# Optimization experiments

Hardware: AMD Instinct MI355X
Metric: run time of the kernel (lower is better)

The kernel has to match this reference:

```python
import jax, jax.numpy as jnp
import numpy as np

N = 50000          # nodes
E = 800000         # edges (before self-loops)
IN_CH = 128
H1, C1 = 8, 32     # layer-1 heads / channels-per-head (concat -> 256)
H2, C2 = 1, 64     # layer-2 (out_channels=64, heads=1)
NEG_SLOPE = 0.2    # PyG GATConv default LeakyReLU slope for attention


def setup_inputs() -> dict:
    key = jax.random.key(0)
    ks = jax.random.split(key, 10)
    x = jax.random.normal(ks[0], (N, IN_CH), dtype=jnp.float32)
    edge_index = jax.random.randint(ks[1], (2, E), 0, N, dtype=jnp.int64)
    s = 0.05
    W1 = jax.random.normal(ks[2], (IN_CH, H1 * C1), dtype=jnp.float32) * s
    a_src1 = jax.random.normal(ks[3], (H1, C1), dtype=jnp.float32) * s
    a_dst1 = jax.random.normal(ks[4], (H1, C1), dtype=jnp.float32) * s
    b1 = jnp.zeros((H1 * C1,), dtype=jnp.float32)
    W2 = jax.random.normal(ks[5], (H1 * C1, H2 * C2), dtype=jnp.float32) * s
    a_src2 = jax.random.normal(ks[6], (H2, C2), dtype=jnp.float32) * s
    a_dst2 = jax.random.normal(ks[7], (H2, C2), dtype=jnp.float32) * s
    b2 = jnp.zeros((H2 * C2,), dtype=jnp.float32)
    return {"x": x, "edge_index": edge_index,
            "W1": W1, "a_src1": a_src1, "a_dst1": a_dst1, "b1": b1,
            "W2": W2, "a_src2": a_src2, "a_dst2": a_dst2, "b2": b2}


def gat_conv(x, src, dst, W, a_src, a_dst, b, heads, ch):
    """PyG GATConv (eval mode): gather -> LeakyReLU attn -> scatter-softmax -> scatter-add."""
    n = x.shape[0]
    h = (x @ W).reshape(n, heads, ch)                     # [N, H, C]
    alpha_s = jnp.einsum('nhc,hc->nh', h, a_src)          # [N, H]
    alpha_d = jnp.einsum('nhc,hc->nh', h, a_dst)
    e = jax.nn.leaky_relu(alpha_s[src] + alpha_d[dst], NEG_SLOPE)  # [E, H]
    # numerically-stable softmax over edges grouped by destination node
    emax = jax.ops.segment_max(e, dst, num_segments=n)
    e = jnp.exp(e - emax[dst])
    denom = jax.ops.segment_sum(e, dst, num_segments=n)
    alpha = e / denom[dst]                                # [E, H]
    out = jax.ops.segment_sum(h[src] * alpha[:, :, None], dst, num_segments=n)  # [N, H, C]
    return out.reshape(n, heads * ch) + b


def reference(x, edge_index, W1, a_src1, a_dst1, b1, W2, a_src2, a_dst2, b2):
    # PyG GATConv adds self-loops by default
    loops = jnp.arange(N, dtype=edge_index.dtype)
    src = jnp.concatenate([edge_index[0], loops])
    dst = jnp.concatenate([edge_index[1], loops])
    h = jax.nn.relu(gat_conv(x, src, dst, W1, a_src1, a_dst1, b1, H1, C1))
    out = jax.nn.relu(gat_conv(h, src, dst, W2, a_src2, a_dst2, b2, H2, C2))
    return out
```

## Files before the change

kernel.cpp:

```cpp
#include <hip/hip_runtime.h>
#include <math.h>

#define NEG_SLOPE 0.2f
__device__ __forceinline__ float leaky(float x) { return fmaxf(x, NEG_SLOPE * x); }

typedef _Float16 f16;
typedef _Float16 f16x4 __attribute__((ext_vector_type(4)));
typedef _Float16 f16x8 __attribute__((ext_vector_type(8)));
typedef float f32x4 __attribute__((ext_vector_type(4)));

__device__ __forceinline__ int kmap(int lh, int e) {
  return (e < 4) ? lh * 4 + e : 16 + lh * 4 + (e - 4);
}

__global__ void k_count(const int* __restrict__ dst, int* __restrict__ deg,
                        int* __restrict__ rank, int E) {
  int e = blockIdx.x * blockDim.x + threadIdx.x;
  if (e < E) {
    int d = dst[e];
    rank[e] = atomicAdd(&deg[d], 1);
  }
}

#define W1_TOT (17 * 4 * 64 * 8)
#define W2_TOT (5 * 8 * 64 * 8)
__global__ __launch_bounds__(256) void k_partial_packw(const int* __restrict__ deg,
    int* __restrict__ part, int n, int nb,
    const float* __restrict__ W1, const float* __restrict__ as1f,
    const float* __restrict__ ad1f, const float* __restrict__ W2,
    const float* __restrict__ as2f, const float* __restrict__ ad2f,
    f16* __restrict__ Wp1, f16* __restrict__ Wp2) {
  if ((int)blockIdx.x < nb) {
    __shared__ int s[256];
    int i = blockIdx.x * 256 + threadIdx.x;
    s[threadIdx.x] = (i < n) ? deg[i] : 0;
    __syncthreads();
    for (int off = 128; off > 0; off >>= 1) {
      if (threadIdx.x < off) s[threadIdx.x] += s[threadIdx.x + off];
      __syncthreads();
    }
    if (threadIdx.x == 0) part[blockIdx.x] = s[0];
  }
  int tid = blockIdx.x * 256 + threadIdx.x;
  if (tid < W1_TOT) {
    int e = tid & 7, l = (tid >> 3) & 63, ks = (tid >> 9) & 3, nt = tid >> 11;
    int lh = l >> 4, li = l & 15;
    int k = ks * 32 + kmap(lh, e);
    float v;
    if (nt < 16) {
      v = W1[k * 256 + nt * 16 + li];
    } else {
      int h = li & 7;
      const float* a = (li < 8) ? (as1f + h * 32) : (ad1f + h * 32);
      v = 0.f;
      for (int j = 0; j < 32; ++j) v += W1[k * 256 + h * 32 + j] * a[j];
    }
    Wp1[tid] = (f16)v;
  } else if (tid < W1_TOT + W2_TOT) {
    int t2 = tid - W1_TOT;
    int e = t2 & 7, l = (t2 >> 3) & 63, ks = (t2 >> 9) & 7, nt = t2 >> 12;
    int lh = l >> 4, li = l & 15;
    int k = ks * 32 + kmap(lh, e);
    float v = 0.f;
    if (nt < 4) {
      v = W2[k * 64 + nt * 16 + li];
    } else if (li == 0) {
      for (int j = 0; j < 64; ++j) v += W2[k * 64 + j] * as2f[j];
    } else if (li == 1) {
      for (int j = 0; j < 64; ++j) v += W2[k * 64 + j] * ad2f[j];
    }
    Wp2[t2] = (f16)v;
  }
}

__global__ __launch_bounds__(256) void k_offs(const int* __restrict__ deg,
                                              const int* __restrict__ part,
                                              int* __restrict__ offs, int n, int nb) {
  __shared__ int ps[256];
  __shared__ int s[256];
  int t = threadIdx.x;
  ps[t] = (t < nb) ? part[t] : 0;
  __syncthreads();
  for (int off = 1; off < 256; off <<= 1) {
    int u = (t >= off) ? ps[t - off] : 0;
    __syncthreads();
    ps[t] += u;
    __syncthreads();
  }
  int base = (blockIdx.x > 0) ? ps[blockIdx.x - 1] : 0;

  int i = blockIdx.x * 256 + t;
  int v = (i < n) ? deg[i] : 0;
  s[t] = v;
  __syncthreads();
  for (int off = 1; off < 256; off <<= 1) {
    int u = (t >= off) ? s[t - off] : 0;
    __syncthreads();
    s[t] += u;
    __syncthreads();
  }
  int excl = base + s[t] - v;
  if (i < n) offs[i] = excl;
  if (i == n - 1) offs[n] = excl + v;
}

__global__ __launch_bounds__(256) void k_fill_gemm1(
    const int* __restrict__ src, const int* __restrict__ dst,
    const int* __restrict__ offs, const int* __restrict__ rank,
    int* __restrict__ col, int E, int fillBlocks,
    const float* __restrict__ x, const f16* __restrict__ Wp1,
    f16* __restrict__ h16, float* __restrict__ as, float* __restrict__ ad,
    int n, int nSlots) {
  if ((int)blockIdx.x < fillBlocks) {
    int e = blockIdx.x * 256 + threadIdx.x;
    if (e >= E) return;
    int d = dst[e];
    col[offs[d] + rank[e]] = src[e];
    return;
  }
  int slot = (blockIdx.x - fillBlocks) * 4 + (threadIdx.x >> 6);
  if (slot >= nSlots) return;
  int half = slot & 1;
  int wid = slot >> 1;
  int lane = threadIdx.x & 63, lh = lane >> 4, li = lane & 15;
  size_t arow = (size_t)min(wid * 16 + li, n - 1);
  f16x8 a[4];
#pragma unroll
  for (int ks = 0; ks < 4; ++ks) {
    float4 lo = *(const float4*)&x[arow * 128 + ks * 32 + lh * 4];
    float4 hi = *(const float4*)&x[arow * 128 + ks * 32 + 16 + lh * 4];
    a[ks][0] = (f16)lo.x; a[ks][1] = (f16)lo.y; a[ks][2] = (f16)lo.z; a[ks][3] = (f16)lo.w;
    a[ks][4] = (f16)hi.x; a[ks][5] = (f16)hi.y; a[ks][6] = (f16)hi.z; a[ks][7] = (f16)hi.w;
  }
  int rbase = wid * 16 + lh * 4;
  int ntBeg = half ? 8 : 0;
  int ntEnd = half ? 17 : 8;
  for (int nt = ntBeg; nt < ntEnd; ++nt) {
    f32x4 acc = {0.f, 0.f, 0.f, 0.f};
#pragma unroll
    for (int ks = 0; ks < 4; ++ks) {
      f16x8 b = *(const f16x8*)&Wp1[((nt * 4 + ks) * 64 + lane) * 8];
      acc = __builtin_amdgcn_mfma_f32_16x16x32_f16(a[ks], b, acc, 0, 0, 0);
    }
    if (nt < 16) {
#pragma unroll
      for (int r = 0; r < 4; ++r) {
        int rr = rbase + r;
        if (rr < n) h16[(size_t)rr * 256 + nt * 16 + li] = (f16)acc[r];
      }
    } else {
#pragma unroll
      for (int r = 0; r < 4; ++r) {
        int rr = rbase + r;
        if (rr < n) {
          if (li < 8) as[(size_t)rr * 8 + li] = acc[r];
          else        ad[(size_t)rr * 8 + (li - 8)] = acc[r];
        }
      }
    }
  }
}

#define RPAD 264
__global__ __launch_bounds__(256) void k_agg1_gemm2(const f16* __restrict__ h16,
    const float* __restrict__ as, const float* __restrict__ ad,
    const int* __restrict__ offs, const int* __restrict__ col,
    const float* __restrict__ b, const f16* __restrict__ Wp2,
    f16* __restrict__ h2, float* __restrict__ as2, float* __restrict__ ad2, int n) {
  __shared__ f16 rs[16][RPAD];
  __shared__ int nextNode;
  int wave = threadIdx.x >> 6;
  int lane = threadIdx.x & 63;
  int head = lane >> 3;
  int c0 = lane * 4;
  if (threadIdx.x == 0) nextNode = 0;
  __syncthreads();

  for (;;) {
    int rl = 0;
    if (lane == 0) rl = atomicAdd(&nextNode, 1);
    rl = __shfl(rl, 0, 64);
    if (rl >= 16) break;
    int node = blockIdx.x * 16 + rl;
    if (node >= n) {
      f16x4 z = {(f16)0.f, (f16)0.f, (f16)0.f, (f16)0.f};
      *(f16x4*)&rs[rl][c0] = z;
      continue;
    }
    node = __builtin_amdgcn_readfirstlane(node);
    int beg = offs[node], end = offs[node + 1];
    float adn = ad[node * 8 + head];

    float denom, ax, ay, az, aw;
    {
      float w = __expf(leaky(as[node * 8 + head] + adn));
      f16x4 g = *(const f16x4*)&h16[(size_t)node * 256 + c0];
      denom = w;
      ax = w * (float)g[0]; ay = w * (float)g[1];
      az = w * (float)g[2]; aw = w * (float)g[3];
    }
    int p = beg;
    for (; p + 8 <= end; p += 8) {
      int s[8];
#pragma unroll
      for (int j = 0; j < 8; ++j) s[j] = col[p + j];
      float e[8];
#pragma unroll
      for (int j = 0; j < 8; ++j) e[j] = as[s[j] * 8 + head];
      f16x4 g[8];
#pragma unroll
      for (int j = 0; j < 8; ++j) g[j] = *(const f16x4*)&h16[(size_t)s[j] * 256 + c0];
      float w[8];
#pragma unroll
      for (int j = 0; j < 8; ++j) w[j] = __expf(leaky(e[j] + adn));
#pragma unroll
      for (int j = 0; j < 8; ++j) {
        denom += w[j];
        ax += w[j] * (float)g[j][0]; ay += w[j] * (float)g[j][1];
        az += w[j] * (float)g[j][2]; aw += w[j] * (float)g[j][3];
      }
    }
    for (; p < end; ++p) {
      int s = col[p];
      float w = __expf(leaky(as[s * 8 + head] + adn));
      f16x4 g = *(const f16x4*)&h16[(size_t)s * 256 + c0];
      denom += w;
      ax += w * (float)g[0]; ay += w * (float)g[1];
      az += w * (float)g[2]; aw += w * (float)g[3];
    }
    float inv = 1.f / denom;
    float4 bv = *(const float4*)&b[c0];
    f16x4 o;
    o[0] = (f16)fmaxf(fmaf(ax, inv, bv.x), 0.f);
    o[1] = (f16)fmaxf(fmaf(ay, inv, bv.y), 0.f);
    o[2] = (f16)fmaxf(fmaf(az, inv, bv.z), 0.f);
    o[3] = (f16)fmaxf(fmaf(aw, inv, bv.w), 0.f);
    *(f16x4*)&rs[rl][c0] = o;
  }
  __syncthreads();

  int lh = lane >> 4, li = lane & 15;
  f16x8 a[8];
#pragma unroll
  for (int ks = 0; ks < 8; ++ks) {
    f16x4 lo = *(const f16x4*)&rs[li][ks * 32 + lh * 4];
    f16x4 hi = *(const f16x4*)&rs[li][ks * 32 + 16 + lh * 4];
    a[ks][0] = lo[0]; a[ks][1] = lo[1]; a[ks][2] = lo[2]; a[ks][3] = lo[3];
    a[ks][4] = hi[0]; a[ks][5] = hi[1]; a[ks][6] = hi[2]; a[ks][7] = hi[3];
  }
  int rbase = blockIdx.x * 16 + lh * 4;
  for (int nt = wave; nt < 5; nt += 4) {
    f32x4 acc = {0.f, 0.f, 0.f, 0.f};
#pragma unroll
    for (int ks = 0; ks < 8; ++ks) {
      f16x8 bb = *(const f16x8*)&Wp2[((nt * 8 + ks) * 64 + lane) * 8];
      acc = __builtin_amdgcn_mfma_f32_16x16x32_f16(a[ks], bb, acc, 0, 0, 0);
    }
    if (nt < 4) {
#pragma unroll
      for (int r = 0; r < 4; ++r) {
        int rr = rbase + r;
        if (rr < n) h2[(size_t)rr * 64 + nt * 16 + li] = (f16)acc[r];
      }
    } else {
#pragma unroll
      for (int r = 0; r < 4; ++r) {
        int rr = rbase + r;
        if (rr < n) {
          if (li == 0) as2[rr] = acc[r];
          else if (li == 1) ad2[rr] = acc[r];
        }
      }
    }
  }
}

__global__ __launch_bounds__(256) void k_agg2(const f16* __restrict__ h2,
    const float* __restrict__ as, const float* __restrict__ ad,
    const int* __restrict__ offs, const int* __restrict__ col,
    const float* __restrict__ b, float* __restrict__ out, int n) {
  int node = blockIdx.x * 4 + (threadIdx.x >> 6);
  if (node >= n) return;
  node = __builtin_amdgcn_readfirstlane(node);
  int lane = threadIdx.x & 63;
  int es = lane >> 4;
  int c = lane & 15;
  int beg = offs[node], end = offs[node + 1];
  int deg = end - beg;
  float adn = ad[node];

  float a0 = 0.f, a1 = 0.f, a2 = 0.f, a3 = 0.f, wsum = 0.f;
  if (es == 0) {
    float w = __expf(leaky(as[node] + adn));
    f16x4 g = *(const f16x4*)&h2[(size_t)node * 64 + c * 4];
    wsum = w;
    a0 = w * (float)g[0]; a1 = w * (float)g[1];
    a2 = w * (float)g[2]; a3 = w * (float)g[3];
  }
  for (int base = 0; base < deg; base += 16) {
    int s[4]; float e[4]; f16x4 g[4]; float w[4];
#pragma unroll
    for (int q = 0; q < 4; ++q) {
      int idx = base + q * 4 + es;
      s[q] = (idx < deg) ? col[beg + idx] : node;
    }
#pragma unroll
    for (int q = 0; q < 4; ++q) e[q] = as[s[q]];
#pragma unroll
    for (int q = 0; q < 4; ++q) g[q] = *(const f16x4*)&h2[(size_t)s[q] * 64 + c * 4];
#pragma unroll
    for (int q = 0; q < 4; ++q) {
      int idx = base + q * 4 + es;
      w[q] = (idx < deg) ? __expf(leaky(e[q] + adn)) : 0.f;
    }
#pragma unroll
    for (int q = 0; q < 4; ++q) {
      wsum += w[q];
      a0 += w[q] * (float)g[q][0]; a1 += w[q] * (float)g[q][1];
      a2 += w[q] * (float)g[q][2]; a3 += w[q] * (float)g[q][3];
    }
  }
  a0 += __shfl_xor(a0, 16, 64); a1 += __shfl_xor(a1, 16, 64);
  a2 += __shfl_xor(a2, 16, 64); a3 += __shfl_xor(a3, 16, 64);
  wsum += __shfl_xor(wsum, 16, 64);
  a0 += __shfl_xor(a0, 32, 64); a1 += __shfl_xor(a1, 32, 64);
  a2 += __shfl_xor(a2, 32, 64); a3 += __shfl_xor(a3, 32, 64);
  wsum += __shfl_xor(wsum, 32, 64);
  if (es == 0) {
    float inv = 1.f / wsum;
    float4 bv = *(const float4*)&b[c * 4];
    f32x4 o;
    o[0] = fmaxf(fmaf(a0, inv, bv.x), 0.f);
    o[1] = fmaxf(fmaf(a1, inv, bv.y), 0.f);
    o[2] = fmaxf(fmaf(a2, inv, bv.z), 0.f);
    o[3] = fmaxf(fmaf(a3, inv, bv.w), 0.f);
    __builtin_nontemporal_store(o, (f32x4*)&out[(size_t)node * 64 + c * 4]);
  }
}

extern "C" void kernel_launch(void* const* d_in, const int* in_sizes, int n_in,
                              void* d_out, int out_size, void* d_ws, size_t ws_size,
                              hipStream_t stream) {
  const float* x      = (const float*)d_in[0];
  const int*   ei     = (const int*)d_in[1];
  const float* W1     = (const float*)d_in[2];
  const float* a_src1 = (const float*)d_in[3];
  const float* a_dst1 = (const float*)d_in[4];
  const float* b1     = (const float*)d_in[5];
  const float* W2     = (const float*)d_in[6];
  const float* a_src2 = (const float*)d_in[7];
  const float* a_dst2 = (const float*)d_in[8];
  const float* b2     = (const float*)d_in[9];

  int N = in_sizes[0] / 128;
  int E = in_sizes[1] / 2;
  const int* srcI = ei;
  const int* dstI = ei + E;
  int nb = (N + 255) / 256;
  int packBlocks = (W1_TOT + W2_TOT + 255) / 256;
  int ppBlocks = nb > packBlocks ? nb : packBlocks;
  int nWaves = (N + 15) / 16;
  int nSlots1 = nWaves * 2;
  int fillBlocks = (E + 255) / 256;
  int gemm1Blocks = (nSlots1 + 3) / 4;
  int nodeBlocks = (N + 3) / 4;
  int aggBlocks = (N + 15) / 16;

  char* ws = (char*)d_ws;
  size_t o = 0;
  auto alloc = [&](size_t bytes) -> void* {
    void* p = ws + o;
    o += (bytes + 255) & ~(size_t)255;
    return p;
  };
  f16*   h1f    = (f16*)alloc((size_t)N * 256 * 2);
  f16*   h2f    = (f16*)alloc((size_t)N * 64 * 2);
  f16*   Wp1    = (f16*)alloc((size_t)W1_TOT * 2);
  f16*   Wp2    = (f16*)alloc((size_t)W2_TOT * 2);
  float* as1    = (float*)alloc((size_t)N * 8 * 4);
  float* ad1    = (float*)alloc((size_t)N * 8 * 4);
  float* as2    = (float*)alloc((size_t)N * 4);
  float* ad2    = (float*)alloc((size_t)N * 4);
  int*   offs   = (int*)alloc((size_t)(N + 1) * 4);
  int*   deg    = (int*)alloc((size_t)N * 4);
  int*   rank   = (int*)alloc((size_t)E * 4);
  int*   col    = (int*)alloc((size_t)E * 4);
  int*   part   = (int*)alloc((size_t)nb * 4);

  hipMemsetAsync(deg, 0, (size_t)N * 4, stream);
  k_count<<<(E + 255) / 256, 256, 0, stream>>>(dstI, deg, rank, E);
  k_partial_packw<<<ppBlocks, 256, 0, stream>>>(deg, part, N, nb,
      W1, a_src1, a_dst1, W2, a_src2, a_dst2, Wp1, Wp2);
  k_offs<<<nb, 256, 0, stream>>>(deg, part, offs, N, nb);

  k_fill_gemm1<<<fillBlocks + gemm1Blocks, 256, 0, stream>>>(
      srcI, dstI, offs, rank, col, E, fillBlocks,
      x, Wp1, h1f, as1, ad1, N, nSlots1);

  k_agg1_gemm2<<<aggBlocks, 256, 0, stream>>>(h1f, as1, ad1, offs, col, b1,
                                              Wp2, h2f, as2, ad2, N);

  k_agg2<<<nodeBlocks, 256, 0, stream>>>(h2f, as2, ad2, offs, col, b2, (float*)d_out, N);
}
```

Baseline: 185.1 us.

## Fuse CSR build stages into one cooperative kernel with grid syncs

Replaces the memset, degree count, partial sum/weight pack, and offset scan launches with a single cooperative kernel of 1024 blocks that uses grid.sync between phases. The goal is to cut several kernel launches and their inter-kernel gaps from the CSR build. It also replaces the per-block atomic work queue in the layer-1 aggregation with a static assignment of four nodes per wave. The trade-off is grid-wide barrier cost and a dependence on cooperative launch fitting all 1024 blocks at once, plus possible load imbalance from skewed node degrees under the static assignment.

```diff
diff --git a/kernel.cpp b/kernel.cpp
--- a/kernel.cpp
+++ b/kernel.cpp
@@ -1,5 +1,8 @@
 #include <hip/hip_runtime.h>
+#include <hip/hip_cooperative_groups.h>
 #include <math.h>
+
+namespace cg = cooperative_groups;
 
 #define NEG_SLOPE 0.2f
 __device__ __forceinline__ float leaky(float x) { return fmaxf(x, NEG_SLOPE * x); }
@@ -13,95 +16,106 @@
   return (e < 4) ? lh * 4 + e : 16 + lh * 4 + (e - 4);
 }
 
-__global__ void k_count(const int* __restrict__ dst, int* __restrict__ deg,
-                        int* __restrict__ rank, int E) {
-  int e = blockIdx.x * blockDim.x + threadIdx.x;
-  if (e < E) {
-    int d = dst[e];
-    rank[e] = atomicAdd(&deg[d], 1);
-  }
-}
-
 #define W1_TOT (17 * 4 * 64 * 8)
 #define W2_TOT (5 * 8 * 64 * 8)
-__global__ __launch_bounds__(256) void k_partial_packw(const int* __restrict__ deg,
-    int* __restrict__ part, int n, int nb,
+
+__global__ __launch_bounds__(256) void k_csr_build(
+    const int* __restrict__ dst, int* __restrict__ deg, int* __restrict__ rank,
+    int* __restrict__ part, int* __restrict__ offs, int n, int E, int nb,
     const float* __restrict__ W1, const float* __restrict__ as1f,
     const float* __restrict__ ad1f, const float* __restrict__ W2,
     const float* __restrict__ as2f, const float* __restrict__ ad2f,
     f16* __restrict__ Wp1, f16* __restrict__ Wp2) {
-  if ((int)blockIdx.x < nb) {
-    __shared__ int s[256];
-    int i = blockIdx.x * 256 + threadIdx.x;
+  cg::grid_group grid = cg::this_grid();
+  __shared__ int s[256];
+  __shared__ int ps[256];
+  int nBlocks = gridDim.x;
+  int gtid = blockIdx.x * 256 + threadIdx.x;
+  int gstride = nBlocks * 256;
+
+  for (int i = gtid; i < n; i += gstride) deg[i] = 0;
+  for (int tid = gtid; tid < W1_TOT + W2_TOT; tid += gstride) {
+    if (tid < W1_TOT) {
+      int e = tid & 7, l = (tid >> 3) & 63, ks = (tid >> 9) & 3, nt = tid >> 11;
+      int lh = l >> 4, li = l & 15;
+      int k = ks * 32 + kmap(lh, e);
+      float v;
+      if (nt < 16) {
+        v = W1[k * 256 + nt * 16 + li];
+      } else {
+        int h = li & 7;
+        const float* a = (li < 8) ? (as1f + h * 32) : (ad1f + h * 32);
+        v = 0.f;
+        for (int j = 0; j < 32; ++j) v += W1[k * 256 + h * 32 + j] * a[j];
+      }
+      Wp1[tid] = (f16)v;
+    } else {
+      int t2 = tid - W1_TOT;
+      int e = t2 & 7, l = (t2 >> 3) & 63, ks = (t2 >> 9) & 7, nt = t2 >> 12;
+      int lh = l >> 4, li = l & 15;
+      int k = ks * 32 + kmap(lh, e);
+      float v = 0.f;
+      if (nt < 4) {
+        v = W2[k * 64 + nt * 16 + li];
+      } else if (li == 0) {
+        for (int j = 0; j < 64; ++j) v += W2[k * 64 + j] * as2f[j];
+      } else if (li == 1) {
+        for (int j = 0; j < 64; ++j) v += W2[k * 64 + j] * ad2f[j];
+      }
+      Wp2[t2] = (f16)v;
+    }
+  }
+  grid.sync();
+
+  for (int e = gtid; e < E; e += gstride) {
+    rank[e] = atomicAdd(&deg[dst[e]], 1);
+  }
+  grid.sync();
+
+  for (int c = blockIdx.x; c < nb; c += nBlocks) {
+    int i = c * 256 + threadIdx.x;
     s[threadIdx.x] = (i < n) ? deg[i] : 0;
     __syncthreads();
     for (int off = 128; off > 0; off >>= 1) {
       if (threadIdx.x < off) s[threadIdx.x] += s[threadIdx.x + off];
       __syncthreads();
     }
-    if (threadIdx.x == 0) part[blockIdx.x] = s[0];
-  }
-  int tid = blockIdx.x * 256 + threadIdx.x;
-  if (tid < W1_TOT) {
-    int e = tid & 7, l = (tid >> 3) & 63, ks = (tid >> 9) & 3, nt = tid >> 11;
-    int lh = l >> 4, li = l & 15;
-    int k = ks * 32 + kmap(lh, e);
-    float v;
-    if (nt < 16) {
-      v = W1[k * 256 + nt * 16 + li];
-    } else {
-      int h = li & 7;
-      const float* a = (li < 8) ? (as1f + h * 32) : (ad1f + h * 32);
-      v = 0.f;
-      for (int j = 0; j < 32; ++j) v += W1[k * 256 + h * 32 + j] * a[j];
-    }
-    Wp1[tid] = (f16)v;
-  } else if (tid < W1_TOT + W2_TOT) {
-    int t2 = tid - W1_TOT;
-    int e = t2 & 7, l = (t2 >> 3) & 63, ks = (t2 >> 9) & 7, nt = t2 >> 12;
-    int lh = l >> 4, li = l & 15;
-    int k = ks * 32 + kmap(lh, e);
-    float v = 0.f;
-    if (nt < 4) {
-      v = W2[k * 64 + nt * 16 + li];
-    } else if (li == 0) {
-      for (int j = 0; j < 64; ++j) v += W2[k * 64 + j] * as2f[j];
-    } else if (li == 1) {
-      for (int j = 0; j < 64; ++j) v += W2[k * 64 + j] * ad2f[j];
-    }
-    Wp2[t2] = (f16)v;
-  }
-}
-
-__global__ __launch_bounds__(256) void k_offs(const int* __restrict__ deg,
-                                              const int* __restrict__ part,
-                                              int* __restrict__ offs, int n, int nb) {
-  __shared__ int ps[256];
-  __shared__ int s[256];
-  int t = threadIdx.x;
-  ps[t] = (t < nb) ? part[t] : 0;
-  __syncthreads();
-  for (int off = 1; off < 256; off <<= 1) {
-    int u = (t >= off) ? ps[t - off] : 0;
+    if (threadIdx.x == 0) part[c] = s[0];
     __syncthreads();
-    ps[t] += u;
+  }
+  grid.sync();
+
+  if (blockIdx.x == 0) {
+    int t = threadIdx.x;
+    int v = (t < nb) ? part[t] : 0;
+    ps[t] = v;
     __syncthreads();
-  }
-  int base = (blockIdx.x > 0) ? ps[blockIdx.x - 1] : 0;
-
-  int i = blockIdx.x * 256 + t;
-  int v = (i < n) ? deg[i] : 0;
-  s[t] = v;
-  __syncthreads();
-  for (int off = 1; off < 256; off <<= 1) {
-    int u = (t >= off) ? s[t - off] : 0;
+    for (int off = 1; off < 256; off <<= 1) {
+      int u = (t >= off) ? ps[t - off] : 0;
+      __syncthreads();
+      ps[t] += u;
+      __syncthreads();
+    }
+    if (t < nb) part[t] = ps[t] - v;
+  }
+  grid.sync();
+
+  for (int c = blockIdx.x; c < nb; c += nBlocks) {
+    int i = c * 256 + threadIdx.x;
+    int v = (i < n) ? deg[i] : 0;
+    s[threadIdx.x] = v;
     __syncthreads();
-    s[t] += u;
+    for (int off = 1; off < 256; off <<= 1) {
+      int u = (threadIdx.x >= off) ? s[threadIdx.x - off] : 0;
+      __syncthreads();
+      s[threadIdx.x] += u;
+      __syncthreads();
+    }
+    int excl = part[c] + s[threadIdx.x] - v;
+    if (i < n) offs[i] = excl;
+    if (i == n - 1) offs[n] = excl + v;
     __syncthreads();
   }
-  int excl = base + s[t] - v;
-  if (i < n) offs[i] = excl;
-  if (i == n - 1) offs[n] = excl + v;
 }
 
 __global__ __launch_bounds__(256) void k_fill_gemm1(
@@ -168,19 +182,13 @@
     const float* __restrict__ b, const f16* __restrict__ Wp2,
     f16* __restrict__ h2, float* __restrict__ as2, float* __restrict__ ad2, int n) {
   __shared__ f16 rs[16][RPAD];
-  __shared__ int nextNode;
   int wave = threadIdx.x >> 6;
   int lane = threadIdx.x & 63;
   int head = lane >> 3;
   int c0 = lane * 4;
-  if (threadIdx.x == 0) nextNode = 0;
-  __syncthreads();
-
-  for (;;) {
-    int rl = 0;
-    if (lane == 0) rl = atomicAdd(&nextNode, 1);
-    rl = __shfl(rl, 0, 64);
-    if (rl >= 16) break;
+
+  for (int i = 0; i < 4; ++i) {
+    int rl = wave * 4 + i;
     int node = blockIdx.x * 16 + rl;
     if (node >= n) {
       f16x4 z = {(f16)0.f, (f16)0.f, (f16)0.f, (f16)0.f};
@@ -357,8 +365,6 @@
   const int* srcI = ei;
   const int* dstI = ei + E;
   int nb = (N + 255) / 256;
-  int packBlocks = (W1_TOT + W2_TOT + 255) / 256;
-  int ppBlocks = nb > packBlocks ? nb : packBlocks;
   int nWaves = (N + 15) / 16;
   int nSlots1 = nWaves * 2;
   int fillBlocks = (E + 255) / 256;
@@ -387,11 +393,17 @@
   int*   col    = (int*)alloc((size_t)E * 4);
   int*   part   = (int*)alloc((size_t)nb * 4);
 
-  hipMemsetAsync(deg, 0, (size_t)N * 4, stream);
-  k_count<<<(E + 255) / 256, 256, 0, stream>>>(dstI, deg, rank, E);
-  k_partial_packw<<<ppBlocks, 256, 0, stream>>>(deg, part, N, nb,
-      W1, a_src1, a_dst1, W2, a_src2, a_dst2, Wp1, Wp2);
-  k_offs<<<nb, 256, 0, stream>>>(deg, part, offs, N, nb);
+  {
+    int coopBlocks = 1024;
+    void* args[] = {
+        (void*)&dstI, (void*)&deg, (void*)&rank, (void*)&part, (void*)&offs,
+        (void*)&N, (void*)&E, (void*)&nb,
+        (void*)&W1, (void*)&a_src1, (void*)&a_dst1,
+        (void*)&W2, (void*)&a_src2, (void*)&a_dst2,
+        (void*)&Wp1, (void*)&Wp2};
+    hipLaunchCooperativeKernel((const void*)k_csr_build, dim3(coopBlocks), dim3(256),
+                               args, 0, stream);
+  }
 
   k_fill_gemm1<<<fillBlocks + gemm1Blocks, 256, 0, stream>>>(
       srcI, dstI, offs, rank, col, E, fillBlocks,
```

New measurement: 568.1 us. +206.9%, slower.

## Merge count with weight packing, compute scan prefix redundantly, use static node assignment

Applied to the files above, without the earlier changes.

The degree-count atomics now run in the same launch as weight packing, and the separate partial-sum pass is removed. Each offset-scan block instead sums all preceding degrees itself, which costs quadratic redundant reads (about nb^2/2 × 256 ints, served from cache). The aggregation kernel replaces its LDS atomic work queue with a fixed four rows per wave. The goal is fewer launches and less synchronization, at the cost of redundant reads and possible wave load imbalance.

```diff
diff --git a/kernel.cpp b/kernel.cpp
--- a/kernel.cpp
+++ b/kernel.cpp
@@ -13,35 +13,22 @@
   return (e < 4) ? lh * 4 + e : 16 + lh * 4 + (e - 4);
 }
 
-__global__ void k_count(const int* __restrict__ dst, int* __restrict__ deg,
-                        int* __restrict__ rank, int E) {
-  int e = blockIdx.x * blockDim.x + threadIdx.x;
-  if (e < E) {
-    int d = dst[e];
-    rank[e] = atomicAdd(&deg[d], 1);
-  }
-}
-
 #define W1_TOT (17 * 4 * 64 * 8)
 #define W2_TOT (5 * 8 * 64 * 8)
-__global__ __launch_bounds__(256) void k_partial_packw(const int* __restrict__ deg,
-    int* __restrict__ part, int n, int nb,
+
+__global__ __launch_bounds__(256) void k_count_packw(
+    const int* __restrict__ dst, int* __restrict__ deg, int* __restrict__ rank,
+    int E, int countBlocks,
     const float* __restrict__ W1, const float* __restrict__ as1f,
     const float* __restrict__ ad1f, const float* __restrict__ W2,
     const float* __restrict__ as2f, const float* __restrict__ ad2f,
     f16* __restrict__ Wp1, f16* __restrict__ Wp2) {
-  if ((int)blockIdx.x < nb) {
-    __shared__ int s[256];
-    int i = blockIdx.x * 256 + threadIdx.x;
-    s[threadIdx.x] = (i < n) ? deg[i] : 0;
-    __syncthreads();
-    for (int off = 128; off > 0; off >>= 1) {
-      if (threadIdx.x < off) s[threadIdx.x] += s[threadIdx.x + off];
-      __syncthreads();
-    }
-    if (threadIdx.x == 0) part[blockIdx.x] = s[0];
-  }
-  int tid = blockIdx.x * 256 + threadIdx.x;
+  if ((int)blockIdx.x < countBlocks) {
+    int e = blockIdx.x * 256 + threadIdx.x;
+    if (e < E) rank[e] = atomicAdd(&deg[dst[e]], 1);
+    return;
+  }
+  int tid = (blockIdx.x - countBlocks) * 256 + threadIdx.x;
   if (tid < W1_TOT) {
     int e = tid & 7, l = (tid >> 3) & 63, ks = (tid >> 9) & 3, nt = tid >> 11;
     int lh = l >> 4, li = l & 15;
@@ -73,23 +60,23 @@
   }
 }
 
-__global__ __launch_bounds__(256) void k_offs(const int* __restrict__ deg,
-                                              const int* __restrict__ part,
-                                              int* __restrict__ offs, int n, int nb) {
-  __shared__ int ps[256];
+__global__ __launch_bounds__(256) void k_offs2(const int* __restrict__ deg,
+                                               int* __restrict__ offs, int n) {
   __shared__ int s[256];
   int t = threadIdx.x;
-  ps[t] = (t < nb) ? part[t] : 0;
+  int c = blockIdx.x;
+  int partial = 0;
+  int prefixN = c * 256;
+  for (int j = t; j < prefixN; j += 256) partial += deg[j];
+  s[t] = partial;
   __syncthreads();
-  for (int off = 1; off < 256; off <<= 1) {
-    int u = (t >= off) ? ps[t - off] : 0;
+  for (int off = 128; off > 0; off >>= 1) {
+    if (t < off) s[t] += s[t + off];
     __syncthreads();
-    ps[t] += u;
-    __syncthreads();
-  }
-  int base = (blockIdx.x > 0) ? ps[blockIdx.x - 1] : 0;
-
-  int i = blockIdx.x * 256 + t;
+  }
+  int base = s[0];
+  __syncthreads();
+  int i = c * 256 + t;
   int v = (i < n) ? deg[i] : 0;
   s[t] = v;
   __syncthreads();
@@ -168,19 +155,13 @@
     const float* __restrict__ b, const f16* __restrict__ Wp2,
     f16* __restrict__ h2, float* __restrict__ as2, float* __restrict__ ad2, int n) {
   __shared__ f16 rs[16][RPAD];
-  __shared__ int nextNode;
   int wave = threadIdx.x >> 6;
   int lane = threadIdx.x & 63;
   int head = lane >> 3;
   int c0 = lane * 4;
-  if (threadIdx.x == 0) nextNode = 0;
-  __syncthreads();
-
-  for (;;) {
-    int rl = 0;
-    if (lane == 0) rl = atomicAdd(&nextNode, 1);
-    rl = __shfl(rl, 0, 64);
-    if (rl >= 16) break;
+
+  for (int i = 0; i < 4; ++i) {
+    int rl = wave * 4 + i;
     int node = blockIdx.x * 16 + rl;
     if (node >= n) {
       f16x4 z = {(f16)0.f, (f16)0.f, (f16)0.f, (f16)0.f};
@@ -357,10 +338,10 @@
   const int* srcI = ei;
   const int* dstI = ei + E;
   int nb = (N + 255) / 256;
-  int packBlocks = (W1_TOT + W2_TOT + 255) / 256;
-  int ppBlocks = nb > packBlocks ? nb : packBlocks;
   int nWaves = (N + 15) / 16;
   int nSlots1 = nWaves * 2;
+  int countBlocks = (E + 255) / 256;
+  int packBlocks = (W1_TOT + W2_TOT + 255) / 256;
   int fillBlocks = (E + 255) / 256;
   int gemm1Blocks = (nSlots1 + 3) / 4;
   int nodeBlocks = (N + 3) / 4;
@@ -385,13 +366,12 @@
   int*   deg    = (int*)alloc((size_t)N * 4);
   int*   rank   = (int*)alloc((size_t)E * 4);
   int*   col    = (int*)alloc((size_t)E * 4);
-  int*   part   = (int*)alloc((size_t)nb * 4);
 
   hipMemsetAsync(deg, 0, (size_t)N * 4, stream);
-  k_count<<<(E + 255) / 256, 256, 0, stream>>>(dstI, deg, rank, E);
-  k_partial_packw<<<ppBlocks, 256, 0, stream>>>(deg, part, N, nb,
+  k_count_packw<<<countBlocks + packBlocks, 256, 0, stream>>>(
+      dstI, deg, rank, E, countBlocks,
       W1, a_src1, a_dst1, W2, a_src2, a_dst2, Wp1, Wp2);
-  k_offs<<<nb, 256, 0, stream>>>(deg, part, offs, N, nb);
+  k_offs2<<<nb, 256, 0, stream>>>(deg, offs, N);
 
   k_fill_gemm1<<<fillBlocks + gemm1Blocks, 256, 0, stream>>>(
       srcI, dstI, offs, rank, col, E, fillBlocks,
```

Result: slower. 206.0 us (+11.3%).
